# Kernel tuning notes

Hardware: AMD Instinct MI355X
Metric: run time of the kernel (lower is better)

The kernel has to match this reference:

```python
import jax, jax.numpy as jnp
import numpy as np

TWO_N, D = 8192, 256
N = TWO_N // 2


def setup_inputs() -> dict:
    key = jax.random.key(0)
    k1, k2 = jax.random.split(key)
    embeddings = jax.random.normal(k1, (TWO_N, D), dtype=jnp.float32)
    pos_mask = jnp.zeros((N, TWO_N), dtype=bool)  # unused by the loss
    neg_mask = jax.random.randint(k2, (N, TWO_N), 0, 2).astype(bool)
    return {"embeddings": embeddings, "pos_mask": pos_mask, "neg_mask": neg_mask}


def reference(embeddings, pos_mask, neg_mask):
    # d[i, j] = <e_i, e_j>  (other_embeddings defaults to embeddings)
    d = jnp.matmul(embeddings, embeddings.T)            # [2N, 2N]
    n = embeddings.shape[0] // 2
    rows = d[:n]                                        # [N, 2N] (only rows 0..N-1 used)
    ap = rows[jnp.arange(n), jnp.arange(n) + n]         # d[i, i+N], shape [N]
    # masked sum_j exp(d[i,j] - ap_i) over negatives, then log(1 + .)
    expm = jnp.exp(rows - ap[:, None])                  # [N, 2N]
    j_all = jnp.log1p(jnp.sum(jnp.where(neg_mask, expm, 0.0), axis=1))  # [N]
    return jnp.mean(j_all)
```

## Files before the change

kernel.cpp:

```cpp
#include <hip/hip_runtime.h>
#include <hip/hip_bf16.h>
#include <math.h>

#define TWO_N 8192
#define NR 4096
#define D 256
#define BM 128
#define BN 128
#define BKT 64
#define LDK 72

typedef __attribute__((ext_vector_type(8))) short bf16x8;
typedef __attribute__((ext_vector_type(4))) float f32x4;

__device__ inline short f2bf(float x) {
  unsigned u = __builtin_bit_cast(unsigned, x);
  u += 0x7fffu + ((u >> 16) & 1u);
  return (short)(u >> 16);
}

__global__ void zero_kernel(double* __restrict__ rowsum) {
  int i = blockIdx.x * blockDim.x + threadIdx.x;
  if (i < NR) rowsum[i] = 0.0;
}

__global__ void ap_kernel(const float* __restrict__ emb, float* __restrict__ ap) {
  const int lane = threadIdx.x & 63;
  const int wid = threadIdx.x >> 6;
  const int i = blockIdx.x * 4 + wid;
  const float4 a = *reinterpret_cast<const float4*>(emb + (size_t)i * D + lane * 4);
  const float4 b = *reinterpret_cast<const float4*>(emb + (size_t)(i + NR) * D + lane * 4);
  float s = a.x * b.x + a.y * b.y + a.z * b.z + a.w * b.w;
#pragma unroll
  for (int off = 32; off >= 1; off >>= 1) s += __shfl_xor(s, off, 64);
  if (lane == 0) ap[i] = s;
}

__global__ __launch_bounds__(256, 2) void fused_mfma(
    const float* __restrict__ emb, const unsigned char* __restrict__ negm,
    const float* __restrict__ ap, double* __restrict__ rowsum) {
  __shared__ short As[BM * LDK];
  __shared__ short Bs[BN * LDK];
  const int t = threadIdx.x;
  const int lane = t & 63;
  const int wid = t >> 6;
  const int wr = wid >> 1;
  const int wc = wid & 1;
  const int bi = blockIdx.y;
  const int bj = blockIdx.x;

  f32x4 acc[4][4] = {};

  const int srow = t >> 2;
  const int schunk = (t & 3) * 16;

  for (int kt = 0; kt < D / BKT; ++kt) {
    const int k0 = kt * BKT;
#pragma unroll
    for (int h = 0; h < 2; ++h) {
      const int r = srow + h * 64;
      {
        const float* g = emb + (size_t)(bi * BM + r) * D + k0 + schunk;
        short tmp[16];
#pragma unroll
        for (int u = 0; u < 4; ++u) {
          float4 v = *reinterpret_cast<const float4*>(g + u * 4);
          tmp[u * 4 + 0] = f2bf(v.x);
          tmp[u * 4 + 1] = f2bf(v.y);
          tmp[u * 4 + 2] = f2bf(v.z);
          tmp[u * 4 + 3] = f2bf(v.w);
        }
#pragma unroll
        for (int u = 0; u < 2; ++u)
          *reinterpret_cast<bf16x8*>(&As[r * LDK + schunk + u * 8]) =
              *reinterpret_cast<bf16x8*>(&tmp[u * 8]);
      }
      {
        const float* g = emb + (size_t)(bj * BN + r) * D + k0 + schunk;
        short tmp[16];
#pragma unroll
        for (int u = 0; u < 4; ++u) {
          float4 v = *reinterpret_cast<const float4*>(g + u * 4);
          tmp[u * 4 + 0] = f2bf(v.x);
          tmp[u * 4 + 1] = f2bf(v.y);
          tmp[u * 4 + 2] = f2bf(v.z);
          tmp[u * 4 + 3] = f2bf(v.w);
        }
#pragma unroll
        for (int u = 0; u < 2; ++u)
          *reinterpret_cast<bf16x8*>(&Bs[r * LDK + schunk + u * 8]) =
              *reinterpret_cast<bf16x8*>(&tmp[u * 8]);
      }
    }
    __syncthreads();
#pragma unroll
    for (int kk = 0; kk < 2; ++kk) {
      bf16x8 af[4], bfr[4];
      const int kof = kk * 32 + (lane >> 4) * 8;
#pragma unroll
      for (int m = 0; m < 4; ++m)
        af[m] = *reinterpret_cast<const bf16x8*>(&As[(wr * 64 + m * 16 + (lane & 15)) * LDK + kof]);
#pragma unroll
      for (int n = 0; n < 4; ++n)
        bfr[n] = *reinterpret_cast<const bf16x8*>(&Bs[(wc * 64 + n * 16 + (lane & 15)) * LDK + kof]);
#pragma unroll
      for (int m = 0; m < 4; ++m)
#pragma unroll
        for (int n = 0; n < 4; ++n)
          acc[m][n] = __builtin_amdgcn_mfma_f32_16x16x32_bf16(af[m], bfr[n], acc[m][n], 0, 0, 0);
    }
    __syncthreads();
  }

  const int g = lane >> 4;
  const int cl = lane & 15;
  double rs[4][4] = {};

#pragma unroll
  for (int m = 0; m < 4; ++m) {
    const int rowbase = bi * BM + wr * 64 + m * 16 + g * 4;
    float apv[4];
#pragma unroll
    for (int r2 = 0; r2 < 4; ++r2) apv[r2] = ap[rowbase + r2];
#pragma unroll
    for (int n = 0; n < 4; ++n) {
      const int col = bj * BN + wc * 64 + n * 16 + cl;
#pragma unroll
      for (int r2 = 0; r2 < 4; ++r2) {
        const unsigned char msk = negm[(size_t)(rowbase + r2) * TWO_N + col];
        const float x = acc[m][n][r2] - apv[r2];
        const float tt = x * 1.44269504088896340736f;
        const float kf = floorf(tt);
        const float mant = exp2f(tt - kf);
        const long long ebits = (long long)(1023 + (int)kf) << 52;
        const double sc = __builtin_bit_cast(double, ebits);
        rs[m][r2] += msk ? (double)mant * sc : 0.0;
      }
    }
  }
#pragma unroll
  for (int m = 0; m < 4; ++m)
#pragma unroll
    for (int r2 = 0; r2 < 4; ++r2) {
      double v = rs[m][r2];
#pragma unroll
      for (int off = 8; off >= 1; off >>= 1) v += __shfl_xor(v, off, 64);
      if (cl == 0) atomicAdd(&rowsum[bi * BM + wr * 64 + m * 16 + g * 4 + r2], v);
    }
}

__global__ void finalize_kernel(const double* __restrict__ rowsum, float* __restrict__ out) {
  __shared__ double red[4];
  const int t = threadIdx.x;
  double s = 0.0;
  for (int i = t; i < NR; i += 256) s += log1p(rowsum[i]);
#pragma unroll
  for (int off = 32; off >= 1; off >>= 1) s += __shfl_xor(s, off, 64);
  if ((t & 63) == 0) red[t >> 6] = s;
  __syncthreads();
  if (t == 0) out[0] = (float)((red[0] + red[1] + red[2] + red[3]) * (1.0 / NR));
}

extern "C" void kernel_launch(void* const* d_in, const int* in_sizes, int n_in,
                              void* d_out, int out_size, void* d_ws, size_t ws_size,
                              hipStream_t stream) {
  const float* emb = (const float*)d_in[0];
  const unsigned char* negm = (const unsigned char*)d_in[2];
  float* out = (float*)d_out;
  float* ap = (float*)d_ws;
  double* rowsum = (double*)((char*)d_ws + 16384);

  zero_kernel<<<dim3(NR / 256), dim3(256), 0, stream>>>(rowsum);
  ap_kernel<<<dim3(NR / 4), dim3(256), 0, stream>>>(emb, ap);
  fused_mfma<<<dim3(TWO_N / BN, NR / BM), dim3(256), 0, stream>>>(emb, negm, ap, rowsum);
  finalize_kernel<<<dim3(1), dim3(256), 0, stream>>>(rowsum, out);
}
```

Measured before the change: 303.3 us.

## Pre-convert embeddings to bf16 and stream tiles with direct global-to-LDS loads

Adds a conversion kernel that writes a bf16 copy of the embeddings once, so the GEMM no longer reloads fp32 data and repeats the conversion in every tile. The tile loads now use global_load_lds to move 16-byte chunks straight into unpadded LDS. It also swizzles the block index across a 1-D grid for cache locality, raises the occupancy hint to 3 blocks per CU, and folds the rowsum zeroing into the ap kernel. The unpadded LDS layout can cause bank conflicts on the fragment reads, and the extra conversion pass adds a launch and a write.

```diff
diff --git a/kernel.cpp b/kernel.cpp
--- a/kernel.cpp
+++ b/kernel.cpp
@@ -1,5 +1,4 @@
 #include <hip/hip_runtime.h>
-#include <hip/hip_bf16.h>
 #include <math.h>
 
 #define TWO_N 8192
@@ -7,24 +6,32 @@
 #define D 256
 #define BM 128
 #define BN 128
-#define BKT 64
-#define LDK 72
+#define BK 64
 
 typedef __attribute__((ext_vector_type(8))) short bf16x8;
 typedef __attribute__((ext_vector_type(4))) float f32x4;
 
-__device__ inline short f2bf(float x) {
+#define AS1V const __attribute__((address_space(1))) void
+#define AS3V __attribute__((address_space(3))) void
+
+__device__ inline unsigned short f2bf(float x) {
   unsigned u = __builtin_bit_cast(unsigned, x);
   u += 0x7fffu + ((u >> 16) & 1u);
-  return (short)(u >> 16);
+  return (unsigned short)(u >> 16);
 }
 
-__global__ void zero_kernel(double* __restrict__ rowsum) {
-  int i = blockIdx.x * blockDim.x + threadIdx.x;
-  if (i < NR) rowsum[i] = 0.0;
+__global__ void cvt_kernel(const float* __restrict__ emb, unsigned short* __restrict__ ebf) {
+  const size_t i = ((size_t)blockIdx.x * 256 + threadIdx.x) * 8;
+  const float4 a = *reinterpret_cast<const float4*>(emb + i);
+  const float4 b = *reinterpret_cast<const float4*>(emb + i + 4);
+  union { unsigned short s[8]; bf16x8 v; } o;
+  o.s[0] = f2bf(a.x); o.s[1] = f2bf(a.y); o.s[2] = f2bf(a.z); o.s[3] = f2bf(a.w);
+  o.s[4] = f2bf(b.x); o.s[5] = f2bf(b.y); o.s[6] = f2bf(b.z); o.s[7] = f2bf(b.w);
+  *reinterpret_cast<bf16x8*>(ebf + i) = o.v;
 }
 
-__global__ void ap_kernel(const float* __restrict__ emb, float* __restrict__ ap) {
+__global__ void ap_zero_kernel(const float* __restrict__ emb, float* __restrict__ ap,
+                               double* __restrict__ rowsum) {
   const int lane = threadIdx.x & 63;
   const int wid = threadIdx.x >> 6;
   const int i = blockIdx.x * 4 + wid;
@@ -33,64 +40,37 @@
   float s = a.x * b.x + a.y * b.y + a.z * b.z + a.w * b.w;
 #pragma unroll
   for (int off = 32; off >= 1; off >>= 1) s += __shfl_xor(s, off, 64);
-  if (lane == 0) ap[i] = s;
+  if (lane == 0) { ap[i] = s; rowsum[i] = 0.0; }
 }
 
-__global__ __launch_bounds__(256, 2) void fused_mfma(
-    const float* __restrict__ emb, const unsigned char* __restrict__ negm,
+__global__ __launch_bounds__(256, 3) void fused_mfma(
+    const unsigned short* __restrict__ ebf, const unsigned char* __restrict__ negm,
     const float* __restrict__ ap, double* __restrict__ rowsum) {
-  __shared__ short As[BM * LDK];
-  __shared__ short Bs[BN * LDK];
+  __shared__ unsigned short As[BM * BK];
+  __shared__ unsigned short Bs[BN * BK];
   const int t = threadIdx.x;
   const int lane = t & 63;
   const int wid = t >> 6;
   const int wr = wid >> 1;
   const int wc = wid & 1;
-  const int bi = blockIdx.y;
-  const int bj = blockIdx.x;
+  const int sw = (blockIdx.x & 7) * 256 + (blockIdx.x >> 3);
+  const int bi = sw >> 6;
+  const int bj = sw & 63;
 
   f32x4 acc[4][4] = {};
 
-  const int srow = t >> 2;
-  const int schunk = (t & 3) * 16;
+  const int srow = lane >> 3;
+  const int scol = (lane & 7) * 8;
 
-  for (int kt = 0; kt < D / BKT; ++kt) {
-    const int k0 = kt * BKT;
+  for (int kt = 0; kt < D / BK; ++kt) {
+    const int k0 = kt * BK;
 #pragma unroll
-    for (int h = 0; h < 2; ++h) {
-      const int r = srow + h * 64;
-      {
-        const float* g = emb + (size_t)(bi * BM + r) * D + k0 + schunk;
-        short tmp[16];
-#pragma unroll
-        for (int u = 0; u < 4; ++u) {
-          float4 v = *reinterpret_cast<const float4*>(g + u * 4);
-          tmp[u * 4 + 0] = f2bf(v.x);
-          tmp[u * 4 + 1] = f2bf(v.y);
-          tmp[u * 4 + 2] = f2bf(v.z);
-          tmp[u * 4 + 3] = f2bf(v.w);
-        }
-#pragma unroll
-        for (int u = 0; u < 2; ++u)
-          *reinterpret_cast<bf16x8*>(&As[r * LDK + schunk + u * 8]) =
-              *reinterpret_cast<bf16x8*>(&tmp[u * 8]);
-      }
-      {
-        const float* g = emb + (size_t)(bj * BN + r) * D + k0 + schunk;
-        short tmp[16];
-#pragma unroll
-        for (int u = 0; u < 4; ++u) {
-          float4 v = *reinterpret_cast<const float4*>(g + u * 4);
-          tmp[u * 4 + 0] = f2bf(v.x);
-          tmp[u * 4 + 1] = f2bf(v.y);
-          tmp[u * 4 + 2] = f2bf(v.z);
-          tmp[u * 4 + 3] = f2bf(v.w);
-        }
-#pragma unroll
-        for (int u = 0; u < 2; ++u)
-          *reinterpret_cast<bf16x8*>(&Bs[r * LDK + schunk + u * 8]) =
-              *reinterpret_cast<bf16x8*>(&tmp[u * 8]);
-      }
+    for (int q = 0; q < 4; ++q) {
+      const int rbase = wid * 32 + q * 8;
+      const unsigned short* gA = ebf + (size_t)(bi * BM + rbase + srow) * D + k0 + scol;
+      const unsigned short* gB = ebf + (size_t)(bj * BN + rbase + srow) * D + k0 + scol;
+      __builtin_amdgcn_global_load_lds((AS1V*)gA, (AS3V*)(As + rbase * BK), 16, 0, 0);
+      __builtin_amdgcn_global_load_lds((AS1V*)gB, (AS3V*)(Bs + rbase * BK), 16, 0, 0);
     }
     __syncthreads();
 #pragma unroll
@@ -99,10 +79,10 @@
       const int kof = kk * 32 + (lane >> 4) * 8;
 #pragma unroll
       for (int m = 0; m < 4; ++m)
-        af[m] = *reinterpret_cast<const bf16x8*>(&As[(wr * 64 + m * 16 + (lane & 15)) * LDK + kof]);
+        af[m] = *reinterpret_cast<const bf16x8*>(&As[(wr * 64 + m * 16 + (lane & 15)) * BK + kof]);
 #pragma unroll
       for (int n = 0; n < 4; ++n)
-        bfr[n] = *reinterpret_cast<const bf16x8*>(&Bs[(wc * 64 + n * 16 + (lane & 15)) * LDK + kof]);
+        bfr[n] = *reinterpret_cast<const bf16x8*>(&Bs[(wc * 64 + n * 16 + (lane & 15)) * BK + kof]);
 #pragma unroll
       for (int m = 0; m < 4; ++m)
 #pragma unroll
@@ -167,11 +147,12 @@
   const float* emb = (const float*)d_in[0];
   const unsigned char* negm = (const unsigned char*)d_in[2];
   float* out = (float*)d_out;
-  float* ap = (float*)d_ws;
-  double* rowsum = (double*)((char*)d_ws + 16384);
+  unsigned short* ebf = (unsigned short*)d_ws;
+  float* ap = (float*)((char*)d_ws + (size_t)TWO_N * D * 2);
+  double* rowsum = (double*)((char*)d_ws + (size_t)TWO_N * D * 2 + 16384);
 
-  zero_kernel<<<dim3(NR / 256), dim3(256), 0, stream>>>(rowsum);
-  ap_kernel<<<dim3(NR / 4), dim3(256), 0, stream>>>(emb, ap);
-  fused_mfma<<<dim3(TWO_N / BN, NR / BM), dim3(256), 0, stream>>>(emb, negm, ap, rowsum);
+  cvt_kernel<<<dim3(TWO_N * D / 8 / 256), dim3(256), 0, stream>>>(emb, ebf);
+  ap_zero_kernel<<<dim3(NR / 4), dim3(256), 0, stream>>>(emb, ap, rowsum);
+  fused_mfma<<<dim3((NR / BM) * (TWO_N / BN)), dim3(256), 0, stream>>>(ebf, negm, ap, rowsum);
   finalize_kernel<<<dim3(1), dim3(256), 0, stream>>>(rowsum, out);
 }
```

Result: faster. 296.9 us (-2.1%).
